# Kernel tuning notes

Measured on AMD Instinct MI355X. Metric: run time of the kernel, lower is better.

Reference implementation:

```python
import jax, jax.numpy as jnp
import numpy as np

D_MODEL = 1024
N_HEADS = 16
D_HEAD = D_MODEL // N_HEADS


def setup_inputs() -> dict:
    key = jax.random.key(0)
    ks = jax.random.split(key, 9)
    s = 1.0 / np.sqrt(D_MODEL)
    x = jax.random.normal(ks[0], (2, 2048, D_MODEL), dtype=jnp.float32)
    Wq = jax.random.uniform(ks[1], (D_MODEL, D_MODEL), jnp.float32, -s, s)
    bq = jax.random.uniform(ks[2], (D_MODEL,), jnp.float32, -s, s)
    Wk = jax.random.uniform(ks[3], (D_MODEL, D_MODEL), jnp.float32, -s, s)
    bk = jax.random.uniform(ks[4], (D_MODEL,), jnp.float32, -s, s)
    Wv = jax.random.uniform(ks[5], (D_MODEL, D_MODEL), jnp.float32, -s, s)
    bv = jax.random.uniform(ks[6], (D_MODEL,), jnp.float32, -s, s)
    Wo = jax.random.uniform(ks[7], (D_MODEL, D_MODEL), jnp.float32, -s, s)
    bo = jax.random.uniform(ks[8], (D_MODEL,), jnp.float32, -s, s)
    return {"x": x, "Wq": Wq, "bq": bq, "Wk": Wk, "bk": bk,
            "Wv": Wv, "bv": bv, "Wo": Wo, "bo": bo}


def reference(x, Wq, bq, Wk, bk, Wv, bv, Wo, bo):
    B, T, _ = x.shape
    # projections: (B, T, d_model) -> (B, H, T, d_head)
    def split_heads(y):
        return y.reshape(B, T, N_HEADS, D_HEAD).transpose(0, 2, 1, 3)
    Q = split_heads(x @ Wq + bq)
    K = split_heads(x @ Wk + bk)
    V = split_heads(x @ Wv + bv)
    scores = jnp.einsum('bhqd,bhkd->bhqk', Q, K) / jnp.sqrt(jnp.float32(D_HEAD))
    causal = jnp.tril(jnp.ones((T, T), dtype=bool))  # allowed positions
    scores = jnp.where(causal, scores, -jnp.inf)
    attn = jax.nn.softmax(scores, axis=-1)
    out = jnp.einsum('bhqk,bhkd->bhqd', attn, V)
    out = out.transpose(0, 2, 1, 3).reshape(B, T, D_MODEL)
    return out @ Wo + bo
```

## Files before the change

kernel.cpp:

```cpp
#include <hip/hip_runtime.h>

typedef unsigned short u16;
typedef unsigned int u32;

#define DM 1024
#define NH 16
#define DH 64
#define BB 2
#define TT 2048

#define SCLQ 0.18033688f

using frag8  = __attribute__((ext_vector_type(8))) short;
using bf16x8 = __attribute__((ext_vector_type(8))) __bf16;
using f32x4  = __attribute__((ext_vector_type(4))) float;

__device__ inline u16 f2bf(float f) {
  union { float f; u32 u; } v; v.f = f;
  u32 r = v.u + 0x7fffu + ((v.u >> 16) & 1u);
  return (u16)(r >> 16);
}

__device__ inline f32x4 mfma_bf16(frag8 a, frag8 b, f32x4 c) {
  return __builtin_amdgcn_mfma_f32_16x16x32_bf16(
      __builtin_bit_cast(bf16x8, a), __builtin_bit_cast(bf16x8, b), c, 0, 0, 0);
}

__device__ inline void gld16(void* lds, const void* g) {
  __builtin_amdgcn_global_load_lds(
      (const __attribute__((address_space(1))) void*)g,
      (__attribute__((address_space(3))) void*)lds, 16, 0, 0);
}

__device__ inline int swi(int row, int chunk) {
  return row * 64 + ((chunk ^ (row & 7)) << 3);
}

__device__ inline int sidx128(int row, int col) {
  return row * 128 + ((((col >> 3) ^ (row & 7)) << 3) | (col & 7));
}

__global__ __launch_bounds__(256) void prep_kernel(
    const float* __restrict__ X, u16* __restrict__ Y,
    const float* __restrict__ W0, const float* __restrict__ W1,
    const float* __restrict__ W2, const float* __restrict__ W3,
    u16* __restrict__ O0, u16* __restrict__ O1,
    u16* __restrict__ O2, u16* __restrict__ O3) {
  int tid = threadIdx.x;
  if (blockIdx.x < 4096) {
    int i = blockIdx.x * 256 + tid;
    float4 v = ((const float4*)X)[i];
    ushort4 o;
    o.x = f2bf(v.x); o.y = f2bf(v.y); o.z = f2bf(v.z); o.w = f2bf(v.w);
    ((ushort4*)Y)[i] = o;
    return;
  }
  int id = blockIdx.x - 4096;
  int z = id >> 8;
  int rem = id & 255;
  const float* W; u16* Ot;
  switch (z) {
    case 0: W = W0; Ot = O0; break;
    case 1: W = W1; Ot = O1; break;
    case 2: W = W2; Ot = O2; break;
    default: W = W3; Ot = O3; break;
  }
  __shared__ u16 Ls[64][72];
  int n0 = (rem & 15) * 64;
  int k0 = (rem >> 4) * 64;
#pragma unroll
  for (int p = 0; p < 4; ++p) {
    int iid = tid + p * 256;
    int row = iid >> 4;
    int c4 = (iid & 15) * 4;
    float4 v = *(const float4*)&W[(size_t)(k0 + row) * DM + n0 + c4];
    ushort4 o; o.x = f2bf(v.x); o.y = f2bf(v.y); o.z = f2bf(v.z); o.w = f2bf(v.w);
    *(ushort4*)&Ls[row][c4] = o;
  }
  __syncthreads();
#pragma unroll
  for (int p = 0; p < 4; ++p) {
    int iid = tid + p * 256;
    int row = iid >> 4;
    int c4 = (iid & 15) * 4;
    ushort4 o;
    o.x = Ls[c4 + 0][row]; o.y = Ls[c4 + 1][row];
    o.z = Ls[c4 + 2][row]; o.w = Ls[c4 + 3][row];
    *(ushort4*)&Ot[(size_t)(n0 + row) * DM + k0 + c4] = o;
  }
}

__global__ __launch_bounds__(256, 3) void gemm_qkv_kernel(
    const u16* __restrict__ A, const u16* __restrict__ Bt,
    const float* __restrict__ b0, const float* __restrict__ b1,
    const float* __restrict__ b2,
    u16* __restrict__ QK, u16* __restrict__ Vt) {
  constexpr int K = 1024;
  constexpr int NT = 32;
  __shared__ u16 sm[24576];
  int tid = threadIdx.x;
  int lane = tid & 63, w = tid >> 6;
  int qd = lane >> 4, ln = lane & 15;
  int wm = (w & 1) * 64, wn = (w >> 1) * 64;
  int lin = blockIdx.y * 24 + blockIdx.x;
  int xcd = lin & 7, j = lin >> 3;
  int m_idx = ((xcd >> 1) << 3) | (j & 7);
  int n_idx = (xcd & 1) * 12 + (j >> 3);
  int m0 = m_idx * 128, n0 = n_idx * 128;
  f32x4 z = {0.f, 0.f, 0.f, 0.f};
  f32x4 acc[4][4];
#pragma unroll
  for (int mi = 0; mi < 4; ++mi)
#pragma unroll
    for (int ni = 0; ni < 4; ++ni) acc[mi][ni] = z;

  const u16* ga = A + (size_t)(m0 + w * 32 + (lane >> 2)) * K + (lane & 3) * 8;
  const u16* gb = Bt + (size_t)(n0 + w * 32 + (lane >> 2)) * K + (lane & 3) * 8;

  auto stage = [&](int t, int buf) {
    u16* Ab = sm + buf * 4096;
    u16* Bb = sm + 12288 + buf * 4096;
    gld16(&Ab[w * 1024],       ga + t * 32);
    gld16(&Ab[w * 1024 + 512], ga + t * 32 + 16 * K);
    gld16(&Bb[w * 1024],       gb + t * 32);
    gld16(&Bb[w * 1024 + 512], gb + t * 32 + 16 * K);
  };

  stage(0, 0);
  stage(1, 1);

  int cur = 0, nbuf = 2;
  for (int t = 0; t < NT; ++t) {
    if (t < NT - 1) {
      asm volatile("s_waitcnt vmcnt(4)" ::: "memory");
    } else {
      asm volatile("s_waitcnt vmcnt(0)" ::: "memory");
    }
    __builtin_amdgcn_sched_barrier(0);
    __builtin_amdgcn_s_barrier();
    if (t + 2 < NT) {
      stage(t + 2, nbuf);
      nbuf = (nbuf == 2) ? 0 : nbuf + 1;
    }
    const u16* Ab = sm + cur * 4096;
    const u16* Bb = sm + 12288 + cur * 4096;
    frag8 af[4], bfr[4];
#pragma unroll
    for (int mi = 0; mi < 4; ++mi)
      af[mi] = *(const frag8*)&Ab[(wm + mi * 16 + ln) * 32 + qd * 8];
#pragma unroll
    for (int ni = 0; ni < 4; ++ni)
      bfr[ni] = *(const frag8*)&Bb[(wn + ni * 16 + ln) * 32 + qd * 8];
    __builtin_amdgcn_s_setprio(1);
#pragma unroll
    for (int mi = 0; mi < 4; ++mi)
#pragma unroll
      for (int ni = 0; ni < 4; ++ni)
        acc[mi][ni] = mfma_bf16(af[mi], bfr[ni], acc[mi][ni]);
    __builtin_amdgcn_s_setprio(0);
    cur = (cur == 2) ? 0 : cur + 1;
  }

  __syncthreads();

  if (n0 < 2048) {
    bool isq = (n0 < 1024);
#pragma unroll
    for (int ni = 0; ni < 4; ++ni) {
      int c_loc = wn + ni * 16 + ln;
      int col = n0 + c_loc;
      float bias = isq ? b0[col] : b1[col - 1024];
#pragma unroll
      for (int mi = 0; mi < 4; ++mi) {
        int rbase = wm + mi * 16 + qd * 4;
#pragma unroll
        for (int r = 0; r < 4; ++r) {
          float v = acc[mi][ni][r] + bias;
          if (isq) v *= SCLQ;
          sm[sidx128(rbase + r, c_loc)] = f2bf(v);
        }
      }
    }
    __syncthreads();
#pragma unroll
    for (int p = 0; p < 8; ++p) {
      int id = p * 256 + tid;
      int tr = id >> 4, cr = id & 15;
      uint4 v = *(const uint4*)&sm[tr * 128 + ((cr ^ (tr & 7)) << 3)];
      *(uint4*)&QK[(size_t)(m0 + tr) * 2048 + n0 + cr * 8] = v;
    }
  } else {
    int b = m0 >> 11, tb = m0 & 2047;
    int n0v = n0 - 2048;
#pragma unroll
    for (int ni = 0; ni < 4; ++ni) {
      int c_loc = wn + ni * 16 + ln;
      float bias = b2[n0v + c_loc];
#pragma unroll
      for (int mi = 0; mi < 4; ++mi) {
        int tbase = wm + mi * 16 + qd * 4;
        u32 lo = ((u32)f2bf(acc[mi][ni][1] + bias) << 16) | f2bf(acc[mi][ni][0] + bias);
        u32 hi = ((u32)f2bf(acc[mi][ni][3] + bias) << 16) | f2bf(acc[mi][ni][2] + bias);
        uint2 pk; pk.x = lo; pk.y = hi;
        int idx = c_loc * 128 + ((((tbase >> 3) ^ (c_loc & 7)) << 3) | (tbase & 7));
        *(uint2*)&sm[idx] = pk;
      }
    }
    __syncthreads();
#pragma unroll
    for (int p = 0; p < 8; ++p) {
      int id = p * 256 + tid;
      int d_loc = id >> 4, tc = id & 15;
      uint4 v = *(const uint4*)&sm[d_loc * 128 + ((tc ^ (d_loc & 7)) << 3)];
      *(uint4*)&Vt[(size_t)(b * 1024 + n0v + d_loc) * 2048 + tb + tc * 8] = v;
    }
  }
}

__global__ __launch_bounds__(256) void gemm_out_kernel(
    const u16* __restrict__ A, const u16* __restrict__ Bt,
    const float* __restrict__ b0, float* __restrict__ Cf) {
  constexpr int K = 1024;
  constexpr int NT = 32;
  __shared__ u16 sm[18432];
  int tid = threadIdx.x;
  int lane = tid & 63, w = tid >> 6;
  int qd = lane >> 4, ln = lane & 15;
  int lin = blockIdx.y * 16 + blockIdx.x;
  int xcd = lin & 7, j = lin >> 3;
  int m_idx = ((xcd >> 1) << 3) | (j & 7);
  int n_idx = ((xcd & 1) << 3) | (j >> 3);
  int m0 = m_idx * 128, n0 = n_idx * 64;
  f32x4 z = {0.f, 0.f, 0.f, 0.f};
  f32x4 acc[2][4];
#pragma unroll
  for (int mi = 0; mi < 2; ++mi)
#pragma unroll
    for (int ni = 0; ni < 4; ++ni) acc[mi][ni] = z;

  const u16* ga = A + (size_t)(m0 + w * 32 + (lane >> 2)) * K + (lane & 3) * 8;
  const u16* gb = Bt + (size_t)(n0 + w * 16 + (lane >> 2)) * K + (lane & 3) * 8;

  auto stage = [&](int t, int buf) {
    u16* Ab = sm + buf * 4096;
    u16* Bb = sm + 12288 + buf * 2048;
    gld16(&Ab[w * 1024],       ga + t * 32);
    gld16(&Ab[w * 1024 + 512], ga + t * 32 + 16 * K);
    gld16(&Bb[w * 512],        gb + t * 32);
  };

  stage(0, 0);
  stage(1, 1);

  int cur = 0, nbuf = 2;
  for (int t = 0; t < NT; ++t) {
    if (t < NT - 1) {
      asm volatile("s_waitcnt vmcnt(3)" ::: "memory");
    } else {
      asm volatile("s_waitcnt vmcnt(0)" ::: "memory");
    }
    __builtin_amdgcn_sched_barrier(0);
    __builtin_amdgcn_s_barrier();
    if (t + 2 < NT) {
      stage(t + 2, nbuf);
      nbuf = (nbuf == 2) ? 0 : nbuf + 1;
    }
    const u16* Ab = sm + cur * 4096;
    const u16* Bb = sm + 12288 + cur * 2048;
    frag8 af[2], bfr[4];
#pragma unroll
    for (int mi = 0; mi < 2; ++mi)
      af[mi] = *(const frag8*)&Ab[(w * 32 + mi * 16 + ln) * 32 + qd * 8];
#pragma unroll
    for (int ni = 0; ni < 4; ++ni)
      bfr[ni] = *(const frag8*)&Bb[(ni * 16 + ln) * 32 + qd * 8];
    __builtin_amdgcn_s_setprio(1);
#pragma unroll
    for (int mi = 0; mi < 2; ++mi)
#pragma unroll
      for (int ni = 0; ni < 4; ++ni)
        acc[mi][ni] = mfma_bf16(af[mi], bfr[ni], acc[mi][ni]);
    __builtin_amdgcn_s_setprio(0);
    cur = (cur == 2) ? 0 : cur + 1;
  }

#pragma unroll
  for (int ni = 0; ni < 4; ++ni) {
    int col = n0 + ni * 16 + ln;
    float bias = b0[col];
#pragma unroll
    for (int mi = 0; mi < 2; ++mi) {
      int row = m0 + w * 32 + mi * 16 + qd * 4;
#pragma unroll
      for (int r = 0; r < 4; ++r)
        Cf[(size_t)(row + r) * 1024 + col] = acc[mi][ni][r] + bias;
    }
  }
}

__global__ __launch_bounds__(256, 4) void flash8_kernel(const u16* __restrict__ QK,
                                                        const u16* __restrict__ Vt,
                                                        u16* __restrict__ O) {
  int lin = blockIdx.y * 32 + blockIdx.x;
  int xcd = lin & 7, u = lin >> 3;
  int a = u & 31, r = u >> 5;
  int bh = (xcd << 2) | r;
  int qt = (r & 1) ? (31 - a) : a;
  int b = bh >> 4, h = bh & 15;
  int q0 = qt * 64;
  __shared__ u16 Ks[2 * 4096];
  __shared__ u16 Vs[2 * 4096];
  __shared__ u16 Ps[4096];
  int tid = threadIdx.x;
  int lane = tid & 63, w = tid >> 6;
  int qd = lane >> 4, ln = lane & 15;

  frag8 qf[2];
#pragma unroll
  for (int kk = 0; kk < 2; ++kk)
    qf[kk] = *(const frag8*)&QK[(size_t)(b * TT + q0 + w * 16 + ln) * 2048 +
                                h * 64 + kk * 32 + qd * 8];

  int lr = lane >> 3, lc = (lane & 7) ^ lr;
  const u16* Kg  = &QK[(size_t)(b * TT + w * 16 + lr) * 2048 + 1024 + h * 64 + lc * 8];
  const u16* Kg2 = Kg + 8 * 2048;
  const u16* Vg  = &Vt[(size_t)(bh * 64 + w * 16 + lr) * 2048 + lc * 8];
  const u16* Vg2 = Vg + 8 * 2048;
  int ldsw = w * 1024;

  int nkt = qt + 1;

  gld16(&Ks[ldsw],       Kg);
  gld16(&Ks[ldsw + 512], Kg2);
  gld16(&Vs[ldsw],       Vg);
  gld16(&Vs[ldsw + 512], Vg2);

  float l = 0.f;
  f32x4 z = {0.f, 0.f, 0.f, 0.f};
  f32x4 o[4] = {z, z, z, z};

  for (int kt = 0; kt < nkt; ++kt) {
    int cur = kt & 1;
    int cb = cur * 4096;
    __syncthreads();

    if (kt + 1 < nkt) {
      int nb = (cur ^ 1) * 4096;
      size_t ko = (size_t)(kt + 1) * 64 * 2048;
      int vo = (kt + 1) * 64;
      gld16(&Ks[nb + ldsw],       Kg + ko);
      gld16(&Ks[nb + ldsw + 512], Kg2 + ko);
      gld16(&Vs[nb + ldsw],       Vg + vo);
      gld16(&Vs[nb + ldsw + 512], Vg2 + vo);
    }

    bool diag = (kt == qt);

    f32x4 s[4] = {z, z, z, z};
    __builtin_amdgcn_s_setprio(1);
#pragma unroll
    for (int mi = 0; mi < 4; ++mi) {
      if (diag && mi > w) continue;
#pragma unroll
      for (int kk = 0; kk < 2; ++kk) {
        frag8 ak = *(const frag8*)&Ks[cb + swi(mi * 16 + ln, 4 * kk + qd)];
        s[mi] = mfma_bf16(ak, qf[kk], s[mi]);
      }
    }
    __builtin_amdgcn_s_setprio(0);

#pragma unroll
    for (int mi = 0; mi < 4; ++mi) {
      int pb = swi(w * 16 + ln, 2 * mi + (qd >> 1)) + (qd & 1) * 4;
      if (diag && mi > w) {
        uint2 zz; zz.x = 0u; zz.y = 0u;
        *(uint2*)&Ps[pb] = zz;
        continue;
      }
      float p0 = __builtin_amdgcn_exp2f(s[mi][0]);
      float p1 = __builtin_amdgcn_exp2f(s[mi][1]);
      float p2 = __builtin_amdgcn_exp2f(s[mi][2]);
      float p3 = __builtin_amdgcn_exp2f(s[mi][3]);
      if (diag && mi == w) {
        p0 = (qd * 4 + 0 <= ln) ? p0 : 0.f;
        p1 = (qd * 4 + 1 <= ln) ? p1 : 0.f;
        p2 = (qd * 4 + 2 <= ln) ? p2 : 0.f;
        p3 = (qd * 4 + 3 <= ln) ? p3 : 0.f;
      }
      l += (p0 + p1) + (p2 + p3);
      u32 u0 = __builtin_bit_cast(u32, p0) + 0x8000u;
      u32 u1 = __builtin_bit_cast(u32, p1) + 0x8000u;
      u32 u2 = __builtin_bit_cast(u32, p2) + 0x8000u;
      u32 u3 = __builtin_bit_cast(u32, p3) + 0x8000u;
      uint2 pk;
      pk.x = __builtin_amdgcn_perm(u1, u0, 0x07060302u);
      pk.y = __builtin_amdgcn_perm(u3, u2, 0x07060302u);
      *(uint2*)&Ps[pb] = pk;
    }

    __builtin_amdgcn_s_setprio(1);
#pragma unroll
    for (int kk = 0; kk < 2; ++kk) {
      if (diag && kk == 1 && w < 2) continue;
      frag8 bp = *(const frag8*)&Ps[swi(w * 16 + ln, 4 * kk + qd)];
#pragma unroll
      for (int mi = 0; mi < 4; ++mi) {
        frag8 av = *(const frag8*)&Vs[cb + swi(mi * 16 + ln, 4 * kk + qd)];
        o[mi] = mfma_bf16(av, bp, o[mi]);
      }
    }
    __builtin_amdgcn_s_setprio(0);
  }

  l += __shfl_xor(l, 16);
  l += __shfl_xor(l, 32);
  float rl = 1.0f / l;

#pragma unroll
  for (int mi = 0; mi < 4; ++mi) {
    ushort4 ov;
    ov.x = f2bf(o[mi][0] * rl); ov.y = f2bf(o[mi][1] * rl);
    ov.z = f2bf(o[mi][2] * rl); ov.w = f2bf(o[mi][3] * rl);
    *(ushort4*)&O[(size_t)(b * TT + q0 + w * 16 + ln) * DM + h * 64 + mi * 16 + qd * 4] = ov;
  }
}

extern "C" void kernel_launch(void* const* d_in, const int* in_sizes, int n_in,
                              void* d_out, int out_size, void* d_ws, size_t ws_size,
                              hipStream_t stream) {
  const float* x  = (const float*)d_in[0];
  const float* Wq = (const float*)d_in[1];
  const float* bq = (const float*)d_in[2];
  const float* Wk = (const float*)d_in[3];
  const float* bk = (const float*)d_in[4];
  const float* Wv = (const float*)d_in[5];
  const float* bv = (const float*)d_in[6];
  const float* Wo = (const float*)d_in[7];
  const float* bo = (const float*)d_in[8];

  char* ws = (char*)d_ws;
  const size_t MB = 1ull << 20;
  u16* xbf  = (u16*)(ws + 0);
  u16* Wcat = (u16*)(ws + 8 * MB);
  u16* Wot  = (u16*)(ws + 14 * MB);
  u16* QKb  = (u16*)(ws + 16 * MB);
  u16* Vtb  = (u16*)(ws + 40 * MB);
  u16* Ob   = (u16*)(ws + 48 * MB);

  prep_kernel<<<5120, 256, 0, stream>>>(
      x, xbf, Wq, Wk, Wv, Wo,
      Wcat, Wcat + 1024 * 1024, Wcat + 2 * 1024 * 1024, Wot);
  gemm_qkv_kernel<<<dim3(24, 32), 256, 0, stream>>>(
      xbf, Wcat, bq, bk, bv, QKb, Vtb);
  flash8_kernel<<<dim3(32, 32), 256, 0, stream>>>(QKb, Vtb, Ob);
  gemm_out_kernel<<<dim3(16, 32), 256, 0, stream>>>(Ob, Wot, bo, (float*)d_out);
}
```

Measured before the change: 175.6 us.

## Enlarge flash attention query tile to 128 rows with 8-wave blocks

The attention kernel now uses 512-thread blocks covering 128 query rows each, so every K/V tile loaded into LDS is shared by twice as many queries. This halves the K/V global traffic per query and halves the grid. The diagonal handling is reworked so that the second sub-tile group skips work on its fully masked tile. In exchange, blocks are larger, LDS use per block is higher, occupancy changes, and the causal workload is coarser, which can worsen load balance.

```diff
diff --git a/kernel.cpp b/kernel.cpp
--- a/kernel.cpp
+++ b/kernel.cpp
@@ -298,22 +298,23 @@
   }
 }
 
-__global__ __launch_bounds__(256, 4) void flash8_kernel(const u16* __restrict__ QK,
+__global__ __launch_bounds__(512, 4) void flash9_kernel(const u16* __restrict__ QK,
                                                         const u16* __restrict__ Vt,
                                                         u16* __restrict__ O) {
-  int lin = blockIdx.y * 32 + blockIdx.x;
+  int lin = blockIdx.x;
   int xcd = lin & 7, u = lin >> 3;
-  int a = u & 31, r = u >> 5;
-  int bh = (xcd << 2) | r;
-  int qt = (r & 1) ? (31 - a) : a;
+  int sl = u >> 5, c = u & 31;
+  int bh = xcd * 4 + ((sl << 1) | (c >> 4));
+  int qt = sl ? (15 - (c & 15)) : (c & 15);
   int b = bh >> 4, h = bh & 15;
-  int q0 = qt * 64;
+  int q0 = qt * 128;
   __shared__ u16 Ks[2 * 4096];
   __shared__ u16 Vs[2 * 4096];
-  __shared__ u16 Ps[4096];
+  __shared__ u16 Ps[8192];
   int tid = threadIdx.x;
   int lane = tid & 63, w = tid >> 6;
   int qd = lane >> 4, ln = lane & 15;
+  int wsl = w >> 2, wl = w & 3;
 
   frag8 qf[2];
 #pragma unroll
@@ -322,18 +323,14 @@
                                 h * 64 + kk * 32 + qd * 8];
 
   int lr = lane >> 3, lc = (lane & 7) ^ lr;
-  const u16* Kg  = &QK[(size_t)(b * TT + w * 16 + lr) * 2048 + 1024 + h * 64 + lc * 8];
-  const u16* Kg2 = Kg + 8 * 2048;
-  const u16* Vg  = &Vt[(size_t)(bh * 64 + w * 16 + lr) * 2048 + lc * 8];
-  const u16* Vg2 = Vg + 8 * 2048;
-  int ldsw = w * 1024;
-
-  int nkt = qt + 1;
-
-  gld16(&Ks[ldsw],       Kg);
-  gld16(&Ks[ldsw + 512], Kg2);
-  gld16(&Vs[ldsw],       Vg);
-  gld16(&Vs[ldsw + 512], Vg2);
+  const u16* Kg = &QK[(size_t)(b * TT + w * 8 + lr) * 2048 + 1024 + h * 64 + lc * 8];
+  const u16* Vg = &Vt[(size_t)(bh * 64 + w * 8 + lr) * 2048 + lc * 8];
+  int ldsw = w * 512;
+
+  int nkt = 2 * qt + 2;
+
+  gld16(&Ks[ldsw], Kg);
+  gld16(&Vs[ldsw], Vg);
 
   float l = 0.f;
   f32x4 z = {0.f, 0.f, 0.f, 0.f};
@@ -348,31 +345,34 @@
       int nb = (cur ^ 1) * 4096;
       size_t ko = (size_t)(kt + 1) * 64 * 2048;
       int vo = (kt + 1) * 64;
-      gld16(&Ks[nb + ldsw],       Kg + ko);
-      gld16(&Ks[nb + ldsw + 512], Kg2 + ko);
-      gld16(&Vs[nb + ldsw],       Vg + vo);
-      gld16(&Vs[nb + ldsw + 512], Vg2 + vo);
-    }
-
-    bool diag = (kt == qt);
+      gld16(&Ks[nb + ldsw], Kg + ko);
+      gld16(&Vs[nb + ldsw], Vg + vo);
+    }
+
+    int jt = kt - 2 * qt;
+    bool dreg = (jt >= 0);
+    bool none = dreg && (jt == 1) && (wsl == 0);
+    bool diag = dreg && (wsl == jt);
 
     f32x4 s[4] = {z, z, z, z};
-    __builtin_amdgcn_s_setprio(1);
-#pragma unroll
-    for (int mi = 0; mi < 4; ++mi) {
-      if (diag && mi > w) continue;
-#pragma unroll
-      for (int kk = 0; kk < 2; ++kk) {
-        frag8 ak = *(const frag8*)&Ks[cb + swi(mi * 16 + ln, 4 * kk + qd)];
-        s[mi] = mfma_bf16(ak, qf[kk], s[mi]);
-      }
-    }
-    __builtin_amdgcn_s_setprio(0);
+    if (!none) {
+      __builtin_amdgcn_s_setprio(1);
+#pragma unroll
+      for (int mi = 0; mi < 4; ++mi) {
+        if (diag && mi > wl) continue;
+#pragma unroll
+        for (int kk = 0; kk < 2; ++kk) {
+          frag8 ak = *(const frag8*)&Ks[cb + swi(mi * 16 + ln, 4 * kk + qd)];
+          s[mi] = mfma_bf16(ak, qf[kk], s[mi]);
+        }
+      }
+      __builtin_amdgcn_s_setprio(0);
+    }
 
 #pragma unroll
     for (int mi = 0; mi < 4; ++mi) {
       int pb = swi(w * 16 + ln, 2 * mi + (qd >> 1)) + (qd & 1) * 4;
-      if (diag && mi > w) {
+      if (none || (diag && mi > wl)) {
         uint2 zz; zz.x = 0u; zz.y = 0u;
         *(uint2*)&Ps[pb] = zz;
         continue;
@@ -381,7 +381,7 @@
       float p1 = __builtin_amdgcn_exp2f(s[mi][1]);
       float p2 = __builtin_amdgcn_exp2f(s[mi][2]);
       float p3 = __builtin_amdgcn_exp2f(s[mi][3]);
-      if (diag && mi == w) {
+      if (diag && mi == wl) {
         p0 = (qd * 4 + 0 <= ln) ? p0 : 0.f;
         p1 = (qd * 4 + 1 <= ln) ? p1 : 0.f;
         p2 = (qd * 4 + 2 <= ln) ? p2 : 0.f;
@@ -398,18 +398,20 @@
       *(uint2*)&Ps[pb] = pk;
     }
 
-    __builtin_amdgcn_s_setprio(1);
-#pragma unroll
-    for (int kk = 0; kk < 2; ++kk) {
-      if (diag && kk == 1 && w < 2) continue;
-      frag8 bp = *(const frag8*)&Ps[swi(w * 16 + ln, 4 * kk + qd)];
-#pragma unroll
-      for (int mi = 0; mi < 4; ++mi) {
-        frag8 av = *(const frag8*)&Vs[cb + swi(mi * 16 + ln, 4 * kk + qd)];
-        o[mi] = mfma_bf16(av, bp, o[mi]);
-      }
-    }
-    __builtin_amdgcn_s_setprio(0);
+    if (!none) {
+      __builtin_amdgcn_s_setprio(1);
+#pragma unroll
+      for (int kk = 0; kk < 2; ++kk) {
+        if (diag && kk == 1 && wl < 2) continue;
+        frag8 bp = *(const frag8*)&Ps[swi(w * 16 + ln, 4 * kk + qd)];
+#pragma unroll
+        for (int mi = 0; mi < 4; ++mi) {
+          frag8 av = *(const frag8*)&Vs[cb + swi(mi * 16 + ln, 4 * kk + qd)];
+          o[mi] = mfma_bf16(av, bp, o[mi]);
+        }
+      }
+      __builtin_amdgcn_s_setprio(0);
+    }
   }
 
   l += __shfl_xor(l, 16);
@@ -452,6 +454,6 @@
       Wcat, Wcat + 1024 * 1024, Wcat + 2 * 1024 * 1024, Wot);
   gemm_qkv_kernel<<<dim3(24, 32), 256, 0, stream>>>(
       xbf, Wcat, bq, bk, bv, QKb, Vtb);
-  flash8_kernel<<<dim3(32, 32), 256, 0, stream>>>(QKb, Vtb, Ob);
+  flash9_kernel<<<512, 512, 0, stream>>>(QKb, Vtb, Ob);
   gemm_out_kernel<<<dim3(16, 32), 256, 0, stream>>>(Ob, Wot, bo, (float*)d_out);
 }
```

After: 187.3 us. +6.7%, slower.
